# Performance work log

Measured on AMD Instinct MI355X. Metric: run time of the kernel, lower is better.

The kernel has to match this reference:

```python
import jax, jax.numpy as jnp
import numpy as np

SIGMA = 5.67e-8  # Stefan-Boltzmann constant
NX = 13
N = NX * NX  # 169 nodes
B = 131072


def _build_matrices(L=0.1, thickness=0.001, board_k=15.0, emis=0.8):
    dx = L / (NX - 1)
    dy = L / (NX - 1)
    GLx = thickness * board_k * dy / dx
    GLy = thickness * board_k * dx / dy
    GR = 2.0 * dx * dy * emis
    iface = {0, NX - 1, NX * NX - 1, NX * NX - NX}
    K = np.zeros((N, N), dtype=np.float32)
    for j in range(NX):
        for i in range(NX):
            idn = i + NX * j
            if idn in iface:
                K[idn, idn] = 1.0
            else:
                gii = 0.0
                if i + 1 < NX:
                    K[idn, idn + 1] = -GLx  # east
                    gii += GLx
                if i - 1 >= 0:
                    K[idn, idn - 1] = -GLx  # west
                    gii += GLx
                if j + 1 < NX:
                    K[idn, idn + NX] = -GLx  # north (original code uses -GLx here too)
                    gii += GLy
                if j - 1 >= 0:
                    K[idn, idn - NX] = -GLx  # south (original code uses -GLx here too)
                    gii += GLy
                K[idn, idn] = gii
    e = np.full(N, GR, dtype=np.float32)
    for t in iface:
        e[t] = 0.0
    return jnp.asarray(K), jnp.asarray(e)


def setup_inputs() -> dict:
    key = jax.random.key(0)
    k1, k2, k3, k4 = jax.random.split(key, 4)
    # realistic temperatures (K) and heat loads (W)
    outputs = 270.0 + 60.0 * jax.random.uniform(k1, (B, NX, NX), dtype=jnp.float32)
    heaters = 0.5 * jax.random.uniform(k2, (B, NX, NX), dtype=jnp.float32)
    interfaces = 0.5 * jax.random.uniform(k3, (B, NX, NX), dtype=jnp.float32)
    Tenv = 270.0 + 30.0 * jax.random.uniform(k4, (B, 1), dtype=jnp.float32)
    K, e_diag = _build_matrices()
    return {"outputs": outputs, "heaters": heaters, "interfaces": interfaces,
            "Tenv": Tenv, "K": K, "e_diag": e_diag}


def reference(outputs, heaters, interfaces, Tenv, K, e_diag):
    b = outputs.shape[0]
    T = outputs.reshape(b, -1)                    # [B, 169]
    Q = heaters.reshape(b, -1) + interfaces.reshape(b, -1)  # [B, 169]
    # original computes K @ T_nodes_x_batch; batch-major equivalent is T @ K^T
    conduction = jnp.einsum('bn,mn->bm', T, K)    # [B, 169]
    radiation = SIGMA * e_diag[None, :] * (T ** 4 - Tenv ** 4)  # Tenv [B,1] broadcasts
    excess = conduction + radiation - Q
    return jnp.mean(jnp.abs(excess))
```

## Files before the change

### kernel.cpp

```cpp
#include <hip/hip_runtime.h>
#include <math.h>


#define SIGMA_F 5.67e-8f

constexpr int NN = 169;
constexpr int BLOCK = 256;
constexpr int GRID = 2048;

__global__ __launch_bounds__(256) void fused_residual_kernel(
    const float* __restrict__ T,
    const float* __restrict__ H,
    const float* __restrict__ F,
    const float* __restrict__ Tenv,
    const float* __restrict__ K,
    const float* __restrict__ Ediag,
    float* __restrict__ partials,
    int total)
{
    __shared__ float sD[NN], sE[NN], sW[NN], sN[NN], sS[NN], sR[NN];
    __shared__ float sred[BLOCK / 64];

    for (int m = (int)threadIdx.x; m < NN; m += BLOCK) {
        const float* row = K + m * NN;
        sD[m] = row[m];
        sE[m] = (m + 1  < NN) ? row[m + 1]  : 0.0f;
        sW[m] = (m >= 1)      ? row[m - 1]  : 0.0f;
        sN[m] = (m + 13 < NN) ? row[m + 13] : 0.0f;
        sS[m] = (m >= 13)     ? row[m - 13] : 0.0f;
        sR[m] = Ediag[m];
    }
    __syncthreads();

    float acc = 0.0f;
    const int stride = gridDim.x * blockDim.x;
    for (int e = blockIdx.x * blockDim.x + threadIdx.x; e < total; e += stride) {
        unsigned ue = (unsigned)e;
        unsigned b  = ue / 169u;
        int m = (int)(ue - b * 169u);

        int es = e - 13; es = es < 0 ? 0 : es;
        int en = e + 13; en = en >= total ? total - 1 : en;
        int ew = e - 1;  ew = ew < 0 ? 0 : ew;
        int ee = e + 1;  ee = ee >= total ? total - 1 : ee;

        float t  = T[e];
        float tS = T[es];
        float tN = T[en];
        float tW = T[ew];
        float tE = T[ee];

        float cond = sD[m] * t + sE[m] * tE + sW[m] * tW + sN[m] * tN + sS[m] * tS;

        float tv  = Tenv[b];
        float t2  = t * t;
        float tv2 = tv * tv;
        float rad = SIGMA_F * sR[m] * (t2 * t2 - tv2 * tv2);

        float q = H[e] + F[e];
        acc += fabsf(cond + rad - q);
    }

    #pragma unroll
    for (int off = 32; off > 0; off >>= 1)
        acc += __shfl_down(acc, off, 64);

    int lane = threadIdx.x & 63;
    int wid  = threadIdx.x >> 6;
    if (lane == 0) sred[wid] = acc;
    __syncthreads();
    if (threadIdx.x == 0) {
        float s = 0.0f;
        #pragma unroll
        for (int w = 0; w < BLOCK / 64; ++w) s += sred[w];
        partials[blockIdx.x] = s;
    }
}

__global__ __launch_bounds__(256) void finalize_kernel(
    const float* __restrict__ partials, int n,
    float* __restrict__ out, float inv_total)
{
    __shared__ float sred[BLOCK / 64];
    float acc = 0.0f;
    for (int i = (int)threadIdx.x; i < n; i += BLOCK) acc += partials[i];
    #pragma unroll
    for (int off = 32; off > 0; off >>= 1)
        acc += __shfl_down(acc, off, 64);
    int lane = threadIdx.x & 63;
    int wid  = threadIdx.x >> 6;
    if (lane == 0) sred[wid] = acc;
    __syncthreads();
    if (threadIdx.x == 0) {
        float s = 0.0f;
        #pragma unroll
        for (int w = 0; w < BLOCK / 64; ++w) s += sred[w];
        out[0] = s * inv_total;
    }
}

extern "C" void kernel_launch(void* const* d_in, const int* in_sizes, int n_in,
                              void* d_out, int out_size, void* d_ws, size_t ws_size,
                              hipStream_t stream) {
    const float* T    = (const float*)d_in[0];
    const float* H    = (const float*)d_in[1];
    const float* F    = (const float*)d_in[2];
    const float* Tenv = (const float*)d_in[3];
    const float* K    = (const float*)d_in[4];
    const float* E    = (const float*)d_in[5];
    float* out      = (float*)d_out;
    float* partials = (float*)d_ws;

    const int total = in_sizes[0];

    int grid = GRID;
    if ((size_t)grid * sizeof(float) > ws_size) grid = (int)(ws_size / sizeof(float));
    if (grid < 1) grid = 1;

    fused_residual_kernel<<<grid, BLOCK, 0, stream>>>(T, H, F, Tenv, K, E, partials, total);

    const float inv_total = 1.0f / (float)total;
    finalize_kernel<<<1, BLOCK, 0, stream>>>(partials, grid, out, inv_total);
}
```

Before: 259.2 us.

## Vectorize stencil residual to four elements per thread with shuffle-shared neighbors

Each thread now handles four consecutive nodes using 16-byte loads of T, H and F, plus unaligned vector loads for the ±13 neighbors. The ±1 neighbors are taken from adjacent lanes with wave shuffles. The per-node K coefficient tables in shared memory are replaced by two scalars read from K and Ediag, with boundary and interface handling derived from the node index. This cuts per-element load instructions and index work, but it assumes K has uniform stencil coefficients. It also keeps a scalar fallback path for the edges of the array.

```diff
diff --git a/kernel.cpp b/kernel.cpp
--- a/kernel.cpp
+++ b/kernel.cpp
@@ -4,11 +4,13 @@
 
 #define SIGMA_F 5.67e-8f
 
-constexpr int NN = 169;
 constexpr int BLOCK = 256;
-constexpr int GRID = 2048;
+constexpr int GRID  = 2048;
 
-__global__ __launch_bounds__(256) void fused_residual_kernel(
+typedef float f4a __attribute__((ext_vector_type(4), aligned(4)));
+typedef float f4b __attribute__((ext_vector_type(4), aligned(16)));
+
+__global__ __launch_bounds__(256) void fused_residual_v2(
     const float* __restrict__ T,
     const float* __restrict__ H,
     const float* __restrict__ F,
@@ -18,55 +20,104 @@
     float* __restrict__ partials,
     int total)
 {
-    __shared__ float sD[NN], sE[NN], sW[NN], sN[NN], sS[NN], sR[NN];
     __shared__ float sred[BLOCK / 64];
 
-    for (int m = (int)threadIdx.x; m < NN; m += BLOCK) {
-        const float* row = K + m * NN;
-        sD[m] = row[m];
-        sE[m] = (m + 1  < NN) ? row[m + 1]  : 0.0f;
-        sW[m] = (m >= 1)      ? row[m - 1]  : 0.0f;
-        sN[m] = (m + 13 < NN) ? row[m + 13] : 0.0f;
-        sS[m] = (m >= 13)     ? row[m - 13] : 0.0f;
-        sR[m] = Ediag[m];
-    }
-    __syncthreads();
+    const float GLx = -K[1 * 169 + 2];
+    const float GRs = SIGMA_F * Ediag[1];
 
+    const int lane = threadIdx.x & 63;
     float acc = 0.0f;
-    const int stride = gridDim.x * blockDim.x;
-    for (int e = blockIdx.x * blockDim.x + threadIdx.x; e < total; e += stride) {
-        unsigned ue = (unsigned)e;
-        unsigned b  = ue / 169u;
-        int m = (int)(ue - b * 169u);
 
-        int es = e - 13; es = es < 0 ? 0 : es;
-        int en = e + 13; en = en >= total ? total - 1 : en;
-        int ew = e - 1;  ew = ew < 0 ? 0 : ew;
-        int ee = e + 1;  ee = ee >= total ? total - 1 : ee;
+    const int gstride = GRID * BLOCK;
+    for (int g = blockIdx.x * BLOCK + threadIdx.x; g * 4 < total; g += gstride) {
+        const int e0 = g * 4;
+        const int waveBase = e0 - lane * 4;
+        const bool fast = (waveBase >= 16) && (waveBase + 64 * 4 + 16 <= total);
 
-        float t  = T[e];
-        float tS = T[es];
-        float tN = T[en];
-        float tW = T[ew];
-        float tE = T[ee];
+        if (fast) {
+            f4b tc = *(const f4b*)(T + e0);
+            f4a tm = *(const f4a*)(T + e0 - 13);
+            f4a tp = *(const f4a*)(T + e0 + 13);
+            f4b hv = *(const f4b*)(H + e0);
+            f4b fv = *(const f4b*)(F + e0);
 
-        float cond = sD[m] * t + sE[m] * tE + sW[m] * tW + sN[m] * tN + sS[m] * tS;
+            float left = __shfl_up(tc.w, 1);
+            if (lane == 0) left = T[e0 - 1];
+            float right = __shfl_down(tc.x, 1);
+            if (lane == 63) right = T[e0 + 4];
 
-        float tv  = Tenv[b];
-        float t2  = t * t;
-        float tv2 = tv * tv;
-        float rad = SIGMA_F * sR[m] * (t2 * t2 - tv2 * tv2);
+            unsigned ue = (unsigned)e0;
+            unsigned b0 = ue / 169u;
+            int m0 = (int)(ue - b0 * 169u);
+            unsigned q13 = (unsigned)m0 / 13u;
+            int i0 = m0 - (int)q13 * 13;
 
-        float q = H[e] + F[e];
-        acc += fabsf(cond + rad - q);
+            float tvA = Tenv[b0];
+            float tvB = tvA;
+            if (m0 >= 166) tvB = Tenv[b0 + 1];
+            float tv4A = (tvA * tvA) * (tvA * tvA);
+            float tv4B = (tvB * tvB) * (tvB * tvB);
+
+            const float tCv[4] = {tc.x, tc.y, tc.z, tc.w};
+            const float tWv[4] = {left, tc.x, tc.y, tc.z};
+            const float tEv[4] = {tc.y, tc.z, tc.w, right};
+            const float tSv[4] = {tm.x, tm.y, tm.z, tm.w};
+            const float tNv[4] = {tp.x, tp.y, tp.z, tp.w};
+            const float hq[4]  = {hv.x + fv.x, hv.y + fv.y, hv.z + fv.z, hv.w + fv.w};
+
+            int m = m0, ii = i0;
+            bool wrapped = false;
+            #pragma unroll
+            for (int j = 0; j < 4; ++j) {
+                float t = tCv[j];
+                bool cE = (ii < 12), cW = (ii > 0), cN = (m < 156), cS = (m >= 13);
+                bool ifc = (m == 0) | (m == 12) | (m == 156) | (m == 168);
+                float s  = (cE ? tEv[j] : 0.0f) + (cW ? tWv[j] : 0.0f)
+                         + (cN ? tNv[j] : 0.0f) + (cS ? tSv[j] : 0.0f);
+                float nn = (cE ? 1.0f : 0.0f) + (cW ? 1.0f : 0.0f)
+                         + (cN ? 1.0f : 0.0f) + (cS ? 1.0f : 0.0f);
+                float t2 = t * t, t4 = t2 * t2;
+                float tv4 = wrapped ? tv4B : tv4A;
+                float ex = ifc ? (t - hq[j])
+                               : (GLx * (nn * t - s) + GRs * (t4 - tv4) - hq[j]);
+                acc += fabsf(ex);
+                ++m; ++ii;
+                if (ii == 13) ii = 0;
+                if (m == 169) { m = 0; ii = 0; wrapped = true; }
+            }
+        } else {
+            #pragma unroll
+            for (int j = 0; j < 4; ++j) {
+                int e = e0 + j;
+                if (e >= total) break;
+                unsigned b = (unsigned)e / 169u;
+                int m = e - (int)b * 169;
+                unsigned q13 = (unsigned)m / 13u;
+                int ii = m - (int)q13 * 13;
+                bool cE = (ii < 12), cW = (ii > 0), cN = (m < 156), cS = (m >= 13);
+                bool ifc = (m == 0) | (m == 12) | (m == 156) | (m == 168);
+                float t  = T[e];
+                float tE = cE ? T[e + 1]  : 0.0f;
+                float tW = cW ? T[e - 1]  : 0.0f;
+                float tN = cN ? T[e + 13] : 0.0f;
+                float tS = cS ? T[e - 13] : 0.0f;
+                float s  = tE + tW + tN + tS;
+                float nn = (float)((int)cE + (int)cW + (int)cN + (int)cS);
+                float tv = Tenv[b];
+                float tv4 = (tv * tv) * (tv * tv);
+                float t2 = t * t, t4 = t2 * t2;
+                float q = H[e] + F[e];
+                float ex = ifc ? (t - q)
+                               : (GLx * (nn * t - s) + GRs * (t4 - tv4) - q);
+                acc += fabsf(ex);
+            }
+        }
     }
 
     #pragma unroll
     for (int off = 32; off > 0; off >>= 1)
         acc += __shfl_down(acc, off, 64);
-
-    int lane = threadIdx.x & 63;
-    int wid  = threadIdx.x >> 6;
+    int wid = threadIdx.x >> 6;
     if (lane == 0) sred[wid] = acc;
     __syncthreads();
     if (threadIdx.x == 0) {
@@ -117,7 +168,7 @@
     if ((size_t)grid * sizeof(float) > ws_size) grid = (int)(ws_size / sizeof(float));
     if (grid < 1) grid = 1;
 
-    fused_residual_kernel<<<grid, BLOCK, 0, stream>>>(T, H, F, Tenv, K, E, partials, total);
+    fused_residual_v2<<<grid, BLOCK, 0, stream>>>(T, H, F, Tenv, K, E, partials, total);
 
     const float inv_total = 1.0f / (float)total;
     finalize_kernel<<<1, BLOCK, 0, stream>>>(partials, grid, out, inv_total);
```

Result: no change. 260.6 us (+0.5%).
